# Optimization experiments

Hardware: AMD Instinct MI355X
Metric: run time of the kernel (lower is better)

Reference implementation:

```python
import jax, jax.numpy as jnp
import numpy as np

STRIDE = 1
PADDING = 1
THRESHOLD = 0.5
NAN_FRAC = 0.05


def _conv(x, k, stride):
    return jax.lax.conv_general_dilated(
        x, k, (stride, stride), 'VALID',
        dimension_numbers=('NCHW', 'OIHW', 'NCHW'))


def setup_inputs() -> dict:
    key = jax.random.key(0)
    k1, k2, k3, k4 = jax.random.split(key, 4)
    B, C, H, W = 16, 128, 128, 128
    OC, KH, KW = 256, 3, 3
    x = jax.random.normal(k1, (B, C, H, W), jnp.float32)
    nan_mask = jax.random.uniform(k2, (B, C, H, W)) < NAN_FRAC
    x = jnp.where(nan_mask, jnp.nan, x)
    kernel = jax.random.normal(k3, (OC, C, KH, KW), jnp.float32) * 0.05
    bias = jax.random.normal(k4, (OC,), jnp.float32) * 0.05
    return {"x": x, "kernel": kernel, "bias": bias}


def reference(x, kernel, bias):
    # NaN-aware conv: per-patch nan stats shared across out_channels.
    p = PADDING
    x = jnp.pad(x, ((0, 0), (0, 0), (p, p), (p, p)))  # zero pad (zeros are valid values)
    mask = jnp.isnan(x)
    x0 = jnp.where(mask, jnp.zeros((), x.dtype), x)
    OC, C, KH, KW = kernel.shape
    total = float(C * KH * KW)
    ones = jnp.ones((1, C, KH, KW), x.dtype)
    maskf = mask.astype(x.dtype)
    nan_count = _conv(maskf, ones, STRIDE)      # [B,1,oh,ow]
    val_sum = _conv(x0, ones, STRIDE)           # sum of non-nan values per patch
    valid = total - nan_count
    patch_mean = val_sum / jnp.maximum(valid, 1.0)
    s1 = _conv(x0, kernel, STRIDE)              # conv with NaNs zeroed
    m = _conv(maskf, kernel, STRIDE)            # sum of kernel weights at NaN positions
    out = s1 + patch_mean * m + bias[None, :, None, None]
    bad = nan_count / total >= THRESHOLD        # includes all-NaN patches
    return jnp.where(bad, jnp.nan, out)
```

## Files before the change

kernel.cpp:

```cpp
#include <hip/hip_runtime.h>


typedef __attribute__((ext_vector_type(8))) short bf16x8;
typedef __attribute__((ext_vector_type(4))) float f32x4;

#define HH 128
#define WW 128
#define CC 128

__device__ __forceinline__ unsigned short f2bf(float f) {
    union { float f; unsigned int i; } v; v.f = f;
    unsigned int u = v.i;
    if ((u & 0x7FFFFFFFu) > 0x7F800000u) return (unsigned short)((u >> 16) | 0x0040u);
    unsigned int r = u + 0x7FFFu + ((u >> 16) & 1u);
    return (unsigned short)(r >> 16);
}
__device__ __forceinline__ unsigned int sel2(unsigned int v, unsigned int pmu) {
    unsigned int lo = v & 0xFFFFu, hi = v >> 16;
    if ((lo & 0x7FFFu) > 0x7F80u) lo = pmu;
    if ((hi & 0x7FFFu) > 0x7F80u) hi = pmu;
    return lo | (hi << 16);
}
__device__ __forceinline__ void gl16(const void* g, void* l) {
    __builtin_amdgcn_global_load_lds(
        (const __attribute__((address_space(1))) unsigned int*)g,
        (__attribute__((address_space(3))) unsigned int*)l, 16, 0, 0);
}
#define SBAR() __builtin_amdgcn_sched_barrier(0)

__global__ void k_transpose_stats(const float* __restrict__ x,
                                  unsigned short* __restrict__ xT,
                                  float* __restrict__ cnt,
                                  float* __restrict__ sum, int b0) {
    __shared__ __align__(16) unsigned short ls[128][136];
    int bh = blockIdx.x;
    int bl = bh >> 7, h = bh & 127;
    int b = b0 + bl;
    int w = threadIdx.x;
    const float* xp = x + ((long)b * CC * HH * WW) + h * WW + w;
    int cntv = 0; float sumv = 0.f;
    for (int c8 = 0; c8 < 16; ++c8) {
        unsigned short s8[8];
        #pragma unroll
        for (int j = 0; j < 8; ++j) {
            float fv = xp[(long)(c8 * 8 + j) * (HH * WW)];
            unsigned int bits = __float_as_uint(fv);
            if ((bits & 0x7FFFFFFFu) > 0x7F800000u) { cntv++; s8[j] = 0x7FC0u; }
            else { sumv += fv; s8[j] = f2bf(fv); }
        }
        uint4 p;
        p.x = (unsigned)s8[0] | ((unsigned)s8[1] << 16);
        p.y = (unsigned)s8[2] | ((unsigned)s8[3] << 16);
        p.z = (unsigned)s8[4] | ((unsigned)s8[5] << 16);
        p.w = (unsigned)s8[6] | ((unsigned)s8[7] << 16);
        *(uint4*)&ls[w][c8 * 8] = p;
    }
    cnt[(bh << 7) + w] = (float)cntv;
    sum[(bh << 7) + w] = sumv;
    __syncthreads();
    unsigned short* xb = xT + ((long)bh << 14);
    int ch = w & 15, pw = w >> 4;
    #pragma unroll
    for (int r = 0; r < 16; ++r) {
        int p = (r << 3) + pw;
        *(uint4*)(xb + (p << 7) + (ch << 3)) = *(const uint4*)&ls[p][ch << 3];
    }
}

__global__ void k_patchmean(const float* __restrict__ cnt, const float* __restrict__ sum,
                            unsigned short* __restrict__ pm) {
    int idx = blockIdx.x * 256 + threadIdx.x;
    int ow = idx & 127, oh = (idx >> 7) & 127, bl = idx >> 14;
    float nc = 0.f, vs = 0.f;
    #pragma unroll
    for (int kh = 0; kh < 3; ++kh) {
        int ih = oh + kh - 1; if (ih < 0 || ih >= HH) continue;
        #pragma unroll
        for (int kw = 0; kw < 3; ++kw) {
            int iw = ow + kw - 1; if (iw < 0 || iw >= WW) continue;
            int p = (((bl << 7) + ih) << 7) + iw;
            nc += cnt[p]; vs += sum[p];
        }
    }
    float pmv = vs / fmaxf(1152.f - nc, 1.f);
    unsigned short r = f2bf(pmv);
    if (nc >= 576.f) r = 0x7FC0u;
    pm[idx] = r;
}

__global__ void k_w2(const float* __restrict__ krn, unsigned short* __restrict__ W2) {
    int e = blockIdx.x * 256 + threadIdx.x;
    int j = e & 7;
    int c2 = (e >> 3) & 3;
    int r = (e >> 5) & 255;
    int kq = (e >> 13) & 3;
    int khw = e >> 15;
    int c = (kq << 5) + ((c2 ^ ((r >> 1) & 3)) << 3) + j;
    W2[e] = f2bf(krn[(r * 128 + c) * 9 + khw]);
}

__global__ __launch_bounds__(256, 4) void k_gemm(
    const unsigned short* __restrict__ xT, const unsigned short* __restrict__ pm,
    const unsigned short* __restrict__ W2, const float* __restrict__ bias,
    float* __restrict__ out, int b0) {
    __shared__ __align__(16) unsigned short lA[2][64 * 32];
    __shared__ __align__(16) unsigned short lB[2][256 * 32];

    int bid = blockIdx.x;
    int ow0 = (bid & 1) << 6;
    int oh  = (bid >> 1) & 127;
    int bl  = bid >> 8;
    int b   = b0 + bl;

    int tid = threadIdx.x;
    int lane = tid & 63, wave = tid >> 6;
    int l15 = lane & 15, quad = lane >> 4;

    int arow = tid >> 2, apart = tid & 3;
    int ow = ow0 + arow;
    unsigned int pmr = pm[(((bl << 7) + oh) << 7) + ow];

    const char* w2base = (const char*)W2;
    int bsrcoff = (wave << 12) + (lane << 4);
    int bdstoff = (wave << 12);

    f32x4 acc[4][4];
    #pragma unroll
    for (int i = 0; i < 4; ++i)
        #pragma unroll
        for (int j = 0; j < 4; ++j) acc[i][j] = (f32x4)0.f;

    auto issueB = [&](int s, unsigned short* lbbuf) {
        const char* src = w2base + ((long)s << 14) + bsrcoff;
        char* dst = (char*)lbbuf + bdstoff;
        #pragma unroll
        for (int i = 0; i < 4; ++i)
            gl16(src + (i << 10), dst + (i << 10));
    };
    auto loadA = [&](int s, uint4& v, unsigned& msk) {
        int khw = s >> 2, kq = s & 3;
        int kh = khw / 3, kw = khw - kh * 3;
        int ih = oh + kh - 1, iw = ow + kw - 1;
        bool valid = ((unsigned)ih < 128u) && ((unsigned)iw < 128u);
        int ihc = ih < 0 ? 0 : (ih > 127 ? 127 : ih);
        int iwc = iw < 0 ? 0 : (iw > 127 ? 127 : iw);
        v = *(const uint4*)(xT + ((((long)((bl << 7) + ihc) << 7) + iwc) << 7)
                            + (kq << 5) + (apart << 3));
        msk = valid ? 0xFFFFFFFFu : 0u;
    };
    auto stageA = [&](uint4 v, unsigned msk, unsigned short* la) {
        v.x &= msk; v.y &= msk; v.z &= msk; v.w &= msk;
        uint4 r0;
        r0.x = sel2(v.x, pmr); r0.y = sel2(v.y, pmr);
        r0.z = sel2(v.z, pmr); r0.w = sel2(v.w, pmr);
        char* dst = (char*)la + (arow << 6) + ((apart ^ ((arow >> 1) & 3)) << 4);
        *(uint4*)dst = r0;
    };
    auto COMPUTE = [&](const unsigned short* la, const unsigned short* lb) {
        int cb = (quad ^ ((l15 >> 1) & 3)) << 4;
        bf16x8 af[4], bfr[4];
        #pragma unroll
        for (int mi = 0; mi < 4; ++mi)
            af[mi] = *(const bf16x8*)((const char*)la + (((mi << 4) + l15) << 6) + cb);
        #pragma unroll
        for (int ni = 0; ni < 4; ++ni)
            bfr[ni] = *(const bf16x8*)((const char*)lb +
                       (((wave << 6) + (ni << 4) + l15) << 6) + cb);
        #pragma unroll
        for (int mi = 0; mi < 4; ++mi)
            #pragma unroll
            for (int ni = 0; ni < 4; ++ni)
                acc[mi][ni] = __builtin_amdgcn_mfma_f32_16x16x32_bf16(
                    af[mi], bfr[ni], acc[mi][ni], 0, 0, 0);
    };

    uint4 av[2]; unsigned am[2];

    issueB(0, lB[0]); SBAR();
    loadA(0, av[0], am[0]); SBAR();
    loadA(1, av[1], am[1]); SBAR();
    asm volatile("s_waitcnt vmcnt(1)" ::: "memory");
    SBAR();
    stageA(av[0], am[0], lA[0]);
    asm volatile("s_waitcnt lgkmcnt(0)" ::: "memory");
    SBAR();
    __builtin_amdgcn_s_barrier();
    SBAR();

    #pragma unroll
    for (int s = 0; s < 36; ++s) {
        const int cur = s & 1, nxt = cur ^ 1;
        if (s < 35) { issueB(s + 1, lB[nxt]); SBAR(); }
        if (s < 34) { loadA(s + 2, av[cur], am[cur]); SBAR(); }
        if (s < 34)      { asm volatile("s_waitcnt vmcnt(5)" ::: "memory"); }
        else if (s == 34){ asm volatile("s_waitcnt vmcnt(4)" ::: "memory"); }
        SBAR();
        if (s < 35) stageA(av[nxt], am[nxt], lA[nxt]);
        COMPUTE(lA[cur], lB[cur]);
        if (s < 35) {
            if (s < 34) { asm volatile("s_waitcnt vmcnt(1) lgkmcnt(0)" ::: "memory"); }
            else        { asm volatile("s_waitcnt vmcnt(0) lgkmcnt(0)" ::: "memory"); }
            SBAR();
            __builtin_amdgcn_s_barrier();
            SBAR();
        }
    }

    #pragma unroll
    for (int ni = 0; ni < 4; ++ni) {
        int oc = (wave << 6) + (ni << 4) + l15;
        float bv = bias[oc];
        float* op = out + ((long)((b << 8) + oc) * 128 + oh) * 128 + ow0;
        #pragma unroll
        for (int mi = 0; mi < 4; ++mi) {
            int og = (mi << 4) + (quad << 2);
            float4 o;
            o.x = acc[mi][ni][0] + bv;
            o.y = acc[mi][ni][1] + bv;
            o.z = acc[mi][ni][2] + bv;
            o.w = acc[mi][ni][3] + bv;
            *(float4*)(op + og) = o;
        }
    }
}

extern "C" void kernel_launch(void* const* d_in, const int* in_sizes, int n_in,
                              void* d_out, int out_size, void* d_ws, size_t ws_size,
                              hipStream_t stream) {
    const float* x    = (const float*)d_in[0];
    const float* krn  = (const float*)d_in[1];
    const float* bias = (const float*)d_in[2];
    float* out = (float*)d_out;

    const size_t W2_BYTES = 294912ull * 2;
    int G = 16;
    while (G > 1) {
        size_t need = W2_BYTES + 256
                    + (size_t)G * (16384ull * 128 * 2)
                    + (size_t)G * (16384ull * 4) * 2
                    + (size_t)G * (16384ull * 2)
                    + 1024;
        if (need <= ws_size) break;
        G >>= 1;
    }

    char* ws = (char*)d_ws;
    size_t off = 0;
    auto carve = [&](size_t bytes) { char* p = ws + off; off += (bytes + 255) & ~255ull; return p; };
    unsigned short* W2  = (unsigned short*)carve(W2_BYTES);
    unsigned short* xT  = (unsigned short*)carve((size_t)G * 16384 * 128 * 2);
    float*          cnt = (float*)carve((size_t)G * 16384 * 4);
    float*          sum = (float*)carve((size_t)G * 16384 * 4);
    unsigned short* pm  = (unsigned short*)carve((size_t)G * 16384 * 2);

    k_w2<<<dim3(1152), dim3(256), 0, stream>>>(krn, W2);
    for (int b0 = 0; b0 < 16; b0 += G) {
        k_transpose_stats<<<dim3(G * 128), dim3(128), 0, stream>>>(x, xT, cnt, sum, b0);
        k_patchmean<<<dim3(G * 64), dim3(256), 0, stream>>>(cnt, sum, pm);
        k_gemm<<<dim3(G * 256), dim3(256), 0, stream>>>(xT, pm, W2, bias, out, b0);
    }
}
```

Baseline: 619.5 us.

## Enlarge GEMM tile to a full output row with 8 waves and simplified A addressing

Each block now covers a full 128-wide output row times 256 output channels using 512 threads arranged as a 2x4 wave grid. This halves the number of times weight tiles are re-read into LDS per output row, and each thread issues fewer B loads. The clamped im2col addressing is replaced by a precomputed base pointer, with nine precomputed border masks. Out-of-range loads are allowed to touch guard regions added around the transposed input in the workspace. The cost is higher LDS use and register pressure per block and fewer blocks in the grid, and the code relies on the guard padding for its unclamped reads.

```diff
diff --git a/kernel.cpp b/kernel.cpp
--- a/kernel.cpp
+++ b/kernel.cpp
@@ -99,30 +99,41 @@
     W2[e] = f2bf(krn[(r * 128 + c) * 9 + khw]);
 }
 
-__global__ __launch_bounds__(256, 4) void k_gemm(
+__global__ __launch_bounds__(512, 6) void k_gemm(
     const unsigned short* __restrict__ xT, const unsigned short* __restrict__ pm,
     const unsigned short* __restrict__ W2, const float* __restrict__ bias,
     float* __restrict__ out, int b0) {
-    __shared__ __align__(16) unsigned short lA[2][64 * 32];
+    __shared__ __align__(16) unsigned short lA[2][128 * 32];
     __shared__ __align__(16) unsigned short lB[2][256 * 32];
 
     int bid = blockIdx.x;
-    int ow0 = (bid & 1) << 6;
-    int oh  = (bid >> 1) & 127;
-    int bl  = bid >> 8;
-    int b   = b0 + bl;
+    int oh = bid & 127, bl = bid >> 7;
+    int b = b0 + bl;
 
     int tid = threadIdx.x;
     int lane = tid & 63, wave = tid >> 6;
+    int wm = wave >> 2, wn = wave & 3;
     int l15 = lane & 15, quad = lane >> 4;
 
     int arow = tid >> 2, apart = tid & 3;
-    int ow = ow0 + arow;
-    unsigned int pmr = pm[(((bl << 7) + oh) << 7) + ow];
+    unsigned int pmr = pm[(((bl << 7) + oh) << 7) + arow];
+
+    const unsigned short* aBase = xT +
+        (((long)((bl << 7) + oh - 1) << 7) + (arow - 1)) * 128 + (apart << 3);
+    unsigned msk9[9];
+    #pragma unroll
+    for (int kh = 0; kh < 3; ++kh) {
+        bool ihok = (unsigned)(oh + kh - 1) < 128u;
+        #pragma unroll
+        for (int kw = 0; kw < 3; ++kw) {
+            bool iwok = (unsigned)(arow + kw - 1) < 128u;
+            msk9[kh * 3 + kw] = (ihok && iwok) ? 0xFFFFFFFFu : 0u;
+        }
+    }
 
     const char* w2base = (const char*)W2;
-    int bsrcoff = (wave << 12) + (lane << 4);
-    int bdstoff = (wave << 12);
+    int bsrcoff = (wave << 11) + (lane << 4);
+    int bdstoff = (wave << 11);
 
     f32x4 acc[4][4];
     #pragma unroll
@@ -133,20 +144,13 @@
     auto issueB = [&](int s, unsigned short* lbbuf) {
         const char* src = w2base + ((long)s << 14) + bsrcoff;
         char* dst = (char*)lbbuf + bdstoff;
-        #pragma unroll
-        for (int i = 0; i < 4; ++i)
-            gl16(src + (i << 10), dst + (i << 10));
-    };
-    auto loadA = [&](int s, uint4& v, unsigned& msk) {
+        gl16(src, dst);
+        gl16(src + 1024, dst + 1024);
+    };
+    auto loadA = [&](int s, uint4& v) {
         int khw = s >> 2, kq = s & 3;
         int kh = khw / 3, kw = khw - kh * 3;
-        int ih = oh + kh - 1, iw = ow + kw - 1;
-        bool valid = ((unsigned)ih < 128u) && ((unsigned)iw < 128u);
-        int ihc = ih < 0 ? 0 : (ih > 127 ? 127 : ih);
-        int iwc = iw < 0 ? 0 : (iw > 127 ? 127 : iw);
-        v = *(const uint4*)(xT + ((((long)((bl << 7) + ihc) << 7) + iwc) << 7)
-                            + (kq << 5) + (apart << 3));
-        msk = valid ? 0xFFFFFFFFu : 0u;
+        v = *(const uint4*)(aBase + (kh * 16384 + kw * 128 + (kq << 5)));
     };
     auto stageA = [&](uint4 v, unsigned msk, unsigned short* la) {
         v.x &= msk; v.y &= msk; v.z &= msk; v.w &= msk;
@@ -161,11 +165,12 @@
         bf16x8 af[4], bfr[4];
         #pragma unroll
         for (int mi = 0; mi < 4; ++mi)
-            af[mi] = *(const bf16x8*)((const char*)la + (((mi << 4) + l15) << 6) + cb);
+            af[mi] = *(const bf16x8*)((const char*)la +
+                      (((wm << 6) + (mi << 4) + l15) << 6) + cb);
         #pragma unroll
         for (int ni = 0; ni < 4; ++ni)
             bfr[ni] = *(const bf16x8*)((const char*)lb +
-                       (((wave << 6) + (ni << 4) + l15) << 6) + cb);
+                       (((wn << 6) + (ni << 4) + l15) << 6) + cb);
         #pragma unroll
         for (int mi = 0; mi < 4; ++mi)
             #pragma unroll
@@ -174,14 +179,14 @@
                     af[mi], bfr[ni], acc[mi][ni], 0, 0, 0);
     };
 
-    uint4 av[2]; unsigned am[2];
+    uint4 av[2];
 
     issueB(0, lB[0]); SBAR();
-    loadA(0, av[0], am[0]); SBAR();
-    loadA(1, av[1], am[1]); SBAR();
+    loadA(0, av[0]); SBAR();
+    loadA(1, av[1]); SBAR();
     asm volatile("s_waitcnt vmcnt(1)" ::: "memory");
     SBAR();
-    stageA(av[0], am[0], lA[0]);
+    stageA(av[0], msk9[0], lA[0]);
     asm volatile("s_waitcnt lgkmcnt(0)" ::: "memory");
     SBAR();
     __builtin_amdgcn_s_barrier();
@@ -191,11 +196,11 @@
     for (int s = 0; s < 36; ++s) {
         const int cur = s & 1, nxt = cur ^ 1;
         if (s < 35) { issueB(s + 1, lB[nxt]); SBAR(); }
-        if (s < 34) { loadA(s + 2, av[cur], am[cur]); SBAR(); }
-        if (s < 34)      { asm volatile("s_waitcnt vmcnt(5)" ::: "memory"); }
-        else if (s == 34){ asm volatile("s_waitcnt vmcnt(4)" ::: "memory"); }
+        if (s < 34) { loadA(s + 2, av[cur]); SBAR(); }
+        if (s < 34)      { asm volatile("s_waitcnt vmcnt(3)" ::: "memory"); }
+        else if (s == 34){ asm volatile("s_waitcnt vmcnt(2)" ::: "memory"); }
         SBAR();
-        if (s < 35) stageA(av[nxt], am[nxt], lA[nxt]);
+        if (s < 35) stageA(av[nxt], msk9[(s + 1) >> 2], lA[nxt]);
         COMPUTE(lA[cur], lB[cur]);
         if (s < 35) {
             if (s < 34) { asm volatile("s_waitcnt vmcnt(1) lgkmcnt(0)" ::: "memory"); }
@@ -208,18 +213,18 @@
 
     #pragma unroll
     for (int ni = 0; ni < 4; ++ni) {
-        int oc = (wave << 6) + (ni << 4) + l15;
+        int oc = (wn << 6) + (ni << 4) + l15;
         float bv = bias[oc];
-        float* op = out + ((long)((b << 8) + oc) * 128 + oh) * 128 + ow0;
+        float* op = out + ((long)((b << 8) + oc) * 128 + oh) * 128;
         #pragma unroll
         for (int mi = 0; mi < 4; ++mi) {
-            int og = (mi << 4) + (quad << 2);
+            int ow0 = (wm << 6) + (mi << 4) + (quad << 2);
             float4 o;
             o.x = acc[mi][ni][0] + bv;
             o.y = acc[mi][ni][1] + bv;
             o.z = acc[mi][ni][2] + bv;
             o.w = acc[mi][ni][3] + bv;
-            *(float4*)(op + og) = o;
+            *(float4*)(op + ow0) = o;
         }
     }
 }
@@ -233,13 +238,14 @@
     float* out = (float*)d_out;
 
     const size_t W2_BYTES = 294912ull * 2;
+    const size_t GUARD = 65536;
     int G = 16;
     while (G > 1) {
-        size_t need = W2_BYTES + 256
+        size_t need = W2_BYTES + 256 + 2 * GUARD
                     + (size_t)G * (16384ull * 128 * 2)
                     + (size_t)G * (16384ull * 4) * 2
                     + (size_t)G * (16384ull * 2)
-                    + 1024;
+                    + 2048;
         if (need <= ws_size) break;
         G >>= 1;
     }
@@ -248,7 +254,9 @@
     size_t off = 0;
     auto carve = [&](size_t bytes) { char* p = ws + off; off += (bytes + 255) & ~255ull; return p; };
     unsigned short* W2  = (unsigned short*)carve(W2_BYTES);
+    carve(GUARD);
     unsigned short* xT  = (unsigned short*)carve((size_t)G * 16384 * 128 * 2);
+    carve(GUARD);
     float*          cnt = (float*)carve((size_t)G * 16384 * 4);
     float*          sum = (float*)carve((size_t)G * 16384 * 4);
     unsigned short* pm  = (unsigned short*)carve((size_t)G * 16384 * 2);
@@ -257,6 +265,6 @@
     for (int b0 = 0; b0 < 16; b0 += G) {
         k_transpose_stats<<<dim3(G * 128), dim3(128), 0, stream>>>(x, xT, cnt, sum, b0);
         k_patchmean<<<dim3(G * 64), dim3(256), 0, stream>>>(cnt, sum, pm);
-        k_gemm<<<dim3(G * 256), dim3(256), 0, stream>>>(xT, pm, W2, bias, out, b0);
-    }
-}
+        k_gemm<<<dim3(G * 128), dim3(512), 0, stream>>>(xT, pm, W2, bias, out, b0);
+    }
+}
```

Result: slower. 1.583 ms (+155.6%).
